# Kernel optimization log

Hardware: AMD Instinct MI355X
Metric: run time of the kernel (lower is better)

Reference implementation:

```python
import jax, jax.numpy as jnp
import numpy as np

EPS = 1e-5

def _layer_norm(x, g, b):
    mu = jnp.mean(x, axis=-1, keepdims=True)
    var = jnp.mean(jnp.square(x - mu), axis=-1, keepdims=True)
    return (x - mu) * jax.lax.rsqrt(var + EPS) * g + b

def setup_inputs() -> dict:
    key = jax.random.key(0)
    ks = jax.random.split(key, 8)
    B, N, M = 4, 2048, 2048
    Dq, Dc = 512, 768
    H, Dh = 8, 64
    inner = H * Dh  # 512
    s = lambda d: 1.0 / np.sqrt(d)
    return {
        "x": jax.random.normal(ks[0], (B, N, Dq), jnp.float32),
        "cond": jax.random.normal(ks[1], (B, M, Dc), jnp.float32),
        "lnx_g": jnp.ones((Dq,), jnp.float32),
        "lnx_b": jnp.zeros((Dq,), jnp.float32),
        "lnc_g": jnp.ones((Dc,), jnp.float32),
        "lnc_b": jnp.zeros((Dc,), jnp.float32),
        "Wq": jax.random.normal(ks[2], (Dq, inner), jnp.float32) * s(Dq),
        "Wk": jax.random.normal(ks[3], (Dc, inner), jnp.float32) * s(Dc),
        "Wv": jax.random.normal(ks[4], (Dc, inner), jnp.float32) * s(Dc),
        "Wo": jax.random.normal(ks[5], (inner, Dq), jnp.float32) * s(inner),
        "bo": jnp.zeros((Dq,), jnp.float32),
        "lnf_g": jnp.ones((Dq,), jnp.float32),
        "lnf_b": jnp.zeros((Dq,), jnp.float32),
    }

def reference(x, cond, lnx_g, lnx_b, lnc_g, lnc_b, Wq, Wk, Wv, Wo, bo, lnf_g, lnf_b):
    H = 8
    B, N, _ = x.shape
    M = cond.shape[1]
    x_orig = x
    xn = _layer_norm(x, lnx_g, lnx_b)
    cn = _layer_norm(cond, lnc_g, lnc_b)
    q = (xn @ Wq).reshape(B, N, H, -1).transpose(0, 2, 1, 3)  # b h n d
    k = (cn @ Wk).reshape(B, M, H, -1).transpose(0, 2, 1, 3)  # b h m d
    v = (cn @ Wv).reshape(B, M, H, -1).transpose(0, 2, 1, 3)
    scale = q.shape[-1] ** -0.5
    sim = jnp.einsum('bhid,bhjd->bhij', q, k) * scale
    attn = jax.nn.softmax(sim, axis=-1)
    out = jnp.einsum('bhij,bhjd->bhid', attn, v)
    out = out.transpose(0, 2, 1, 3).reshape(B, N, -1)  # b n (h d)
    out = out @ Wo + bo
    out = out + x_orig  # residual=True
    return _layer_norm(out, lnf_g, lnf_b)
```

## Files before the change

### kernel.cpp

```cpp
#include <hip/hip_runtime.h>
#include <hip/hip_bf16.h>
#include <math.h>

#define BB 4
#define NN 2048
#define MM 2048
#define DQ 512
#define DC 768
#define NH 8
#define DH 64
#define INNER 512
#define KVS 1024

typedef short bf16x8 __attribute__((ext_vector_type(8)));
typedef float f32x4  __attribute__((ext_vector_type(4)));

__device__ inline short fbf(float f) {
    __hip_bfloat16 h = __float2bfloat16(f);
    return __builtin_bit_cast(short, h);
}

__device__ inline void gld16(const void* gptr, void* lds_uniform_base) {
    __builtin_amdgcn_global_load_lds(
        (const __attribute__((address_space(1))) void*)gptr,
        (__attribute__((address_space(3))) void*)lds_uniform_base, 16, 0, 0);
}

__global__ __launch_bounds__(256) void prep_k(
    const float* __restrict__ x, const float* __restrict__ cond,
    const float* __restrict__ gx, const float* __restrict__ bx_,
    const float* __restrict__ gc, const float* __restrict__ bc,
    short* __restrict__ xn, short* __restrict__ cn,
    const float* __restrict__ Wq, const float* __restrict__ Wk,
    const float* __restrict__ Wv, const float* __restrict__ Wo,
    short* __restrict__ Wqt, short* __restrict__ Wkvt, short* __restrict__ Wot)
{
    const int bxid = blockIdx.x;
    const int t = threadIdx.x;

    if (bxid < 16384) {
        const int which = bxid >> 13;
        const int row   = bxid & 8191;
        const float* in = which ? cond : x;
        const float* g  = which ? gc : gx;
        const float* bb = which ? bc : bx_;
        short* out      = which ? cn : xn;
        const int D     = which ? DC : DQ;

        const float* xr = in + (size_t)row * D;
        float s = 0.f, s2 = 0.f;
        for (int d = t; d < D; d += 256) {
            float v = xr[d];
            s += v; s2 += v * v;
        }
        __shared__ float red[2][4];
        #pragma unroll
        for (int off = 32; off; off >>= 1) {
            s  += __shfl_down(s,  off, 64);
            s2 += __shfl_down(s2, off, 64);
        }
        const int wave = t >> 6, lane = t & 63;
        if (lane == 0) { red[0][wave] = s; red[1][wave] = s2; }
        __syncthreads();
        if (t == 0) {
            float ts = red[0][0] + red[0][1] + red[0][2] + red[0][3];
            float t2 = red[1][0] + red[1][1] + red[1][2] + red[1][3];
            float mu = ts / (float)D;
            float var = t2 / (float)D - mu * mu;
            red[0][0] = mu;
            red[1][0] = rsqrtf(var + 1e-5f);
        }
        __syncthreads();
        const float mu = red[0][0], rstd = red[1][0];
        short* o = out + (size_t)row * D;
        for (int d = t; d < D; d += 256)
            o[d] = fbf((xr[d] - mu) * rstd * g[d] + bb[d]);
    } else {
        const int tb = bxid - 16384;
        const int y = tb >> 4;
        const int n0 = (tb & 15) * 32;
        const float* W; short* Wt; int K, k0;
        if (y < 16)      { W = Wq; Wt = Wqt;  K = DQ; k0 = y * 32; }
        else if (y < 40) { W = Wk; Wt = Wkvt; K = DC; k0 = (y - 16) * 32; }
        else if (y < 64) { W = Wv; Wt = Wkvt + (size_t)512 * DC; K = DC; k0 = (y - 40) * 32; }
        else             { W = Wo; Wt = Wot;  K = DQ; k0 = (y - 64) * 32; }

        __shared__ float tile[32][33];
        const int r = t >> 3, c4 = (t & 7) * 4;
        float4 vv = *(const float4*)&W[(size_t)(k0 + r) * 512 + n0 + c4];
        tile[c4 + 0][r] = vv.x; tile[c4 + 1][r] = vv.y;
        tile[c4 + 2][r] = vv.z; tile[c4 + 3][r] = vv.w;
        __syncthreads();
        short4 sv;
        sv.x = fbf(tile[r][c4 + 0]); sv.y = fbf(tile[r][c4 + 1]);
        sv.z = fbf(tile[r][c4 + 2]); sv.w = fbf(tile[r][c4 + 3]);
        *(short4*)&Wt[(size_t)(n0 + r) * K + k0 + c4] = sv;
    }
}

__global__ __launch_bounds__(256) void layernorm_res_f32(
    const short* __restrict__ ob, const float* __restrict__ x,
    const float* __restrict__ g, const float* __restrict__ b,
    float* __restrict__ out)
{
    const int row = blockIdx.x;
    const int t = threadIdx.x;
    const size_t base = (size_t)row * DQ;
    float v0, v1;
    {
        unsigned u0 = (unsigned)(unsigned short)ob[base + t];
        unsigned u1 = (unsigned)(unsigned short)ob[base + t + 256];
        v0 = __builtin_bit_cast(float, u0 << 16) + x[base + t];
        v1 = __builtin_bit_cast(float, u1 << 16) + x[base + t + 256];
    }
    float s = v0 + v1, s2 = v0 * v0 + v1 * v1;
    __shared__ float red[2][4];
    #pragma unroll
    for (int off = 32; off; off >>= 1) {
        s  += __shfl_down(s,  off, 64);
        s2 += __shfl_down(s2, off, 64);
    }
    const int wave = t >> 6, lane = t & 63;
    if (lane == 0) { red[0][wave] = s; red[1][wave] = s2; }
    __syncthreads();
    if (t == 0) {
        float ts = red[0][0] + red[0][1] + red[0][2] + red[0][3];
        float t2 = red[1][0] + red[1][1] + red[1][2] + red[1][3];
        float mu = ts / (float)DQ;
        float var = t2 / (float)DQ - mu * mu;
        red[0][0] = mu;
        red[1][0] = rsqrtf(var + 1e-5f);
    }
    __syncthreads();
    const float mu = red[0][0], rstd = red[1][0];
    out[base + t]       = (v0 - mu) * rstd * g[t]       + b[t];
    out[base + t + 256] = (v1 - mu) * rstd * g[t + 256] + b[t + 256];
}

#define GBK 32

__global__ __launch_bounds__(256) void qkv_gemm(
    const short* __restrict__ xn, const short* __restrict__ cn,
    const short* __restrict__ Wqt, const short* __restrict__ Wkvt,
    short* __restrict__ qb, short* __restrict__ kvb, float qsc)
{
    const short* A; const short* Bt; short* outp; int K, Nout, n0; float sc;
    if (blockIdx.x < 4) {
        A = xn; Bt = Wqt; outp = qb; K = DQ; Nout = 512;
        n0 = blockIdx.x * 128; sc = qsc;
    } else {
        A = cn; Bt = Wkvt; outp = kvb; K = DC; Nout = 1024;
        n0 = (blockIdx.x - 4) * 128; sc = 1.f;
    }
    __shared__ short As[128 * GBK];
    __shared__ short Bs[128 * GBK];
    const int t = threadIdx.x;
    const int w = t >> 6, lane = t & 63;
    const int quad = lane >> 4, l16 = lane & 15;
    const int m0 = blockIdx.y * 128;
    const int wm = (w >> 1) * 64, wn = (w & 1) * 64;

    f32x4 acc[4][4];
    #pragma unroll
    for (int i = 0; i < 4; ++i)
        #pragma unroll
        for (int j = 0; j < 4; ++j) acc[i][j] = (f32x4){0.f, 0.f, 0.f, 0.f};

    for (int kt = 0; kt < K; kt += GBK) {
        __syncthreads();
        #pragma unroll
        for (int i = 0; i < 2; ++i) {
            const int j = w * 2 + i;
            const int c = j * 64 + lane;
            gld16(&A[(size_t)(m0 + (c >> 2)) * K + kt + (c & 3) * 8],
                  (char*)As + j * 1024);
            gld16(&Bt[(size_t)(n0 + (c >> 2)) * K + kt + (c & 3) * 8],
                  (char*)Bs + j * 1024);
        }
        __syncthreads();

        bf16x8 af[4], bfr[4];
        #pragma unroll
        for (int mt = 0; mt < 4; ++mt)
            af[mt] = *(bf16x8*)&As[(wm + mt * 16 + l16) * GBK + quad * 8];
        #pragma unroll
        for (int nt = 0; nt < 4; ++nt)
            bfr[nt] = *(bf16x8*)&Bs[(wn + nt * 16 + l16) * GBK + quad * 8];
        #pragma unroll
        for (int mt = 0; mt < 4; ++mt)
            #pragma unroll
            for (int nt = 0; nt < 4; ++nt)
                acc[mt][nt] = __builtin_amdgcn_mfma_f32_16x16x32_bf16(
                    af[mt], bfr[nt], acc[mt][nt], 0, 0, 0);
    }

    #pragma unroll
    for (int mt = 0; mt < 4; ++mt)
        #pragma unroll
        for (int r = 0; r < 4; ++r) {
            const int m = m0 + wm + mt * 16 + quad * 4 + r;
            #pragma unroll
            for (int nt = 0; nt < 4; ++nt) {
                const int n = n0 + wn + nt * 16 + l16;
                outp[(size_t)m * Nout + n] = fbf(acc[mt][nt][r] * sc);
            }
        }
}

__global__ __launch_bounds__(256) void oproj_gemm(
    const short* __restrict__ A, const short* __restrict__ Bt,
    short* __restrict__ outb, const float* __restrict__ bias)
{
    const int K = INNER, Nout = INNER;
    __shared__ short As[128 * GBK];
    __shared__ short Bs[64 * GBK];
    const int t = threadIdx.x;
    const int w = t >> 6, lane = t & 63;
    const int quad = lane >> 4, l16 = lane & 15;
    const int m0 = blockIdx.y * 128, n0 = blockIdx.x * 64;
    const int wm = (w >> 1) * 64, wn = (w & 1) * 32;

    f32x4 acc[4][2];
    #pragma unroll
    for (int i = 0; i < 4; ++i)
        #pragma unroll
        for (int j = 0; j < 2; ++j) acc[i][j] = (f32x4){0.f, 0.f, 0.f, 0.f};

    for (int kt = 0; kt < K; kt += GBK) {
        __syncthreads();
        #pragma unroll
        for (int i = 0; i < 2; ++i) {
            const int j = w * 2 + i;
            const int c = j * 64 + lane;
            gld16(&A[(size_t)(m0 + (c >> 2)) * K + kt + (c & 3) * 8],
                  (char*)As + j * 1024);
        }
        {
            const int c = w * 64 + lane;
            gld16(&Bt[(size_t)(n0 + (c >> 2)) * K + kt + (c & 3) * 8],
                  (char*)Bs + w * 1024);
        }
        __syncthreads();

        bf16x8 af[4], bfr[2];
        #pragma unroll
        for (int mt = 0; mt < 4; ++mt)
            af[mt] = *(bf16x8*)&As[(wm + mt * 16 + l16) * GBK + quad * 8];
        #pragma unroll
        for (int nt = 0; nt < 2; ++nt)
            bfr[nt] = *(bf16x8*)&Bs[(wn + nt * 16 + l16) * GBK + quad * 8];
        #pragma unroll
        for (int mt = 0; mt < 4; ++mt)
            #pragma unroll
            for (int nt = 0; nt < 2; ++nt)
                acc[mt][nt] = __builtin_amdgcn_mfma_f32_16x16x32_bf16(
                    af[mt], bfr[nt], acc[mt][nt], 0, 0, 0);
    }

    #pragma unroll
    for (int mt = 0; mt < 4; ++mt)
        #pragma unroll
        for (int r = 0; r < 4; ++r) {
            const int m = m0 + wm + mt * 16 + quad * 4 + r;
            #pragma unroll
            for (int nt = 0; nt < 2; ++nt) {
                const int n = n0 + wn + nt * 16 + l16;
                outb[(size_t)m * Nout + n] = fbf(acc[mt][nt][r] + bias[n]);
            }
        }
}

#define QT 128
#define JT 64
#define KSTR 72
#define MH (MM / 2)
#define NIT (MH / JT)

__global__ __launch_bounds__(512) void attention_mfma(
    const short* __restrict__ q, const short* __restrict__ kv,
    short* __restrict__ o)
{
    const int b = blockIdx.z, h = blockIdx.y;
    const int i0 = blockIdx.x * QT;
    const int t = threadIdx.x;
    const int wave = t >> 6, lane = t & 63;
    const int w4 = wave & 3, hh = wave >> 2;
    const int quad = lane >> 4, l16 = lane & 15;

    __shared__ __align__(16) char smem[73728];
    typedef short KT[2][64][KSTR];
    KT* Ks = (KT*)smem;
    KT* Vt = (KT*)(smem + 36864);
    float (*Obuf)[32][68] = (float(*)[32][68])(smem);
    float (*Lbuf)[32]     = (float(*)[32])(smem + 34816);

    bf16x8 qf[2][2];
    #pragma unroll
    for (int it = 0; it < 2; ++it) {
        const int row = i0 + w4 * 32 + it * 16 + l16;
        const short* qp = &q[((size_t)(b * NN + row)) * INNER + h * DH];
        qf[it][0] = *(const bf16x8*)&qp[quad * 8];
        qf[it][1] = *(const bf16x8*)&qp[32 + quad * 8];
    }

    f32x4 Oa[2][4];
    f32x4 La[2];
    #pragma unroll
    for (int it = 0; it < 2; ++it) {
        La[it] = (f32x4){0.f, 0.f, 0.f, 0.f};
        #pragma unroll
        for (int dt = 0; dt < 4; ++dt) Oa[it][dt] = (f32x4){0.f, 0.f, 0.f, 0.f};
    }

    const bf16x8 ones8 = {(short)0x3F80, (short)0x3F80, (short)0x3F80, (short)0x3F80,
                          (short)0x3F80, (short)0x3F80, (short)0x3F80, (short)0x3F80};

    const int tt = t & 255, th = t >> 8;
    const int kjj = tt >> 3, kdq = (tt & 7) * 8;
    const int vjp = tt & 31, vd0 = (tt >> 5) * 8;

    const int jl0 = 2 * vjp;
    const int vcol = (jl0 >> 5) * 32 + (((jl0 >> 2) & 3) * 8)
                   + (((jl0 >> 4) & 1) * 4) + (jl0 & 3);

    const short* kp0 = kv + ((size_t)(b * MM + th * MH + kjj))      * KVS + h * DH + kdq;
    const short* kp1 = kv + ((size_t)(b * MM + th * MH + kjj + 32)) * KVS + h * DH + kdq;
    const short* vp0 = kv + ((size_t)(b * MM + th * MH + jl0))      * KVS + 512 + h * DH + vd0;
    const short* vp1 = vp0 + KVS;

    bf16x8 ka, kb2, va, vb;
    auto load = [&]() {
        ka  = *(const bf16x8*)kp0;
        kb2 = *(const bf16x8*)kp1;
        va  = *(const bf16x8*)vp0;
        vb  = *(const bf16x8*)vp1;
        kp0 += (size_t)JT * KVS; kp1 += (size_t)JT * KVS;
        vp0 += (size_t)JT * KVS; vp1 += (size_t)JT * KVS;
    };
    auto store = [&](int pb) {
        *(bf16x8*)&Ks[pb][th][kjj][kdq]      = ka;
        *(bf16x8*)&Ks[pb][th][kjj + 32][kdq] = kb2;
        #pragma unroll
        for (int i = 0; i < 8; ++i) {
            short2 pr; pr.x = va[i]; pr.y = vb[i];
            *(short2*)&Vt[pb][th][vd0 + i][vcol] = pr;
        }
    };

    load(); store(0);
    __syncthreads();

    for (int itr = 0; itr < NIT; ++itr) {
        const int p = itr & 1;
        const bool more = (itr + 1 < NIT);
        if (more) load();

        #pragma unroll
        for (int cc = 0; cc < 2; ++cc) {
            f32x4 Sc[2][2];
            #pragma unroll
            for (int jtl = 0; jtl < 2; ++jtl) {
                const int jt = cc * 2 + jtl;
                bf16x8 kf0 = *(bf16x8*)&Ks[p][hh][jt * 16 + l16][quad * 8];
                bf16x8 kf1 = *(bf16x8*)&Ks[p][hh][jt * 16 + l16][32 + quad * 8];
                #pragma unroll
                for (int it = 0; it < 2; ++it) {
                    f32x4 c = (f32x4){0.f, 0.f, 0.f, 0.f};
                    c = __builtin_amdgcn_mfma_f32_16x16x32_bf16(kf0, qf[it][0], c, 0, 0, 0);
                    c = __builtin_amdgcn_mfma_f32_16x16x32_bf16(kf1, qf[it][1], c, 0, 0, 0);
                    Sc[jtl][it] = c;
                }
            }

            bf16x8 p8[2];
            #pragma unroll
            for (int it = 0; it < 2; ++it) {
                const float e0 = exp2f(Sc[0][it][0]), e1 = exp2f(Sc[0][it][1]);
                const float e2 = exp2f(Sc[0][it][2]), e3 = exp2f(Sc[0][it][3]);
                const float f0 = exp2f(Sc[1][it][0]), f1 = exp2f(Sc[1][it][1]);
                const float f2 = exp2f(Sc[1][it][2]), f3 = exp2f(Sc[1][it][3]);
                uint4 pk;
                pk.x = __builtin_amdgcn_perm(__builtin_bit_cast(unsigned, e1),
                                             __builtin_bit_cast(unsigned, e0), 0x07060302u);
                pk.y = __builtin_amdgcn_perm(__builtin_bit_cast(unsigned, e3),
                                             __builtin_bit_cast(unsigned, e2), 0x07060302u);
                pk.z = __builtin_amdgcn_perm(__builtin_bit_cast(unsigned, f1),
                                             __builtin_bit_cast(unsigned, f0), 0x07060302u);
                pk.w = __builtin_amdgcn_perm(__builtin_bit_cast(unsigned, f3),
                                             __builtin_bit_cast(unsigned, f2), 0x07060302u);
                p8[it] = __builtin_bit_cast(bf16x8, pk);
            }

            #pragma unroll
            for (int dt = 0; dt < 4; ++dt) {
                bf16x8 vb8 = *(bf16x8*)&Vt[p][hh][dt * 16 + l16][cc * 32 + quad * 8];
                Oa[0][dt] = __builtin_amdgcn_mfma_f32_16x16x32_bf16(p8[0], vb8, Oa[0][dt], 0, 0, 0);
                Oa[1][dt] = __builtin_amdgcn_mfma_f32_16x16x32_bf16(p8[1], vb8, Oa[1][dt], 0, 0, 0);
            }
            La[0] = __builtin_amdgcn_mfma_f32_16x16x32_bf16(p8[0], ones8, La[0], 0, 0, 0);
            La[1] = __builtin_amdgcn_mfma_f32_16x16x32_bf16(p8[1], ones8, La[1], 0, 0, 0);
        }

        if (more) store(p ^ 1);
        __syncthreads();
    }

    if (wave >= 4) {
        #pragma unroll
        for (int it = 0; it < 2; ++it) {
            #pragma unroll
            for (int r = 0; r < 4; ++r) {
                const int qr = it * 16 + quad * 4 + r;
                #pragma unroll
                for (int dt = 0; dt < 4; ++dt)
                    Obuf[w4][qr][dt * 16 + l16] = Oa[it][dt][r];
                if (l16 == 0) Lbuf[w4][qr] = La[it][r];
            }
        }
    }
    __syncthreads();
    if (wave < 4) {
        #pragma unroll
        for (int it = 0; it < 2; ++it) {
            #pragma unroll
            for (int r = 0; r < 4; ++r) {
                const int qr = it * 16 + quad * 4 + r;
                const float ltot = La[it][r] + Lbuf[w4][qr];
                const float inv = 1.f / ltot;
                const int row = i0 + w4 * 32 + qr;
                #pragma unroll
                for (int dt = 0; dt < 4; ++dt) {
                    const float val = Oa[it][dt][r] + Obuf[w4][qr][dt * 16 + l16];
                    o[((size_t)(b * NN + row)) * INNER + h * DH + dt * 16 + l16] =
                        fbf(val * inv);
                }
            }
        }
    }
}

extern "C" void kernel_launch(void* const* d_in, const int* in_sizes, int n_in,
                              void* d_out, int out_size, void* d_ws, size_t ws_size,
                              hipStream_t stream)
{
    const float* x     = (const float*)d_in[0];
    const float* cond  = (const float*)d_in[1];
    const float* lnx_g = (const float*)d_in[2];
    const float* lnx_b = (const float*)d_in[3];
    const float* lnc_g = (const float*)d_in[4];
    const float* lnc_b = (const float*)d_in[5];
    const float* Wq    = (const float*)d_in[6];
    const float* Wk    = (const float*)d_in[7];
    const float* Wv    = (const float*)d_in[8];
    const float* Wo    = (const float*)d_in[9];
    const float* bo    = (const float*)d_in[10];
    const float* lnf_g = (const float*)d_in[11];
    const float* lnf_b = (const float*)d_in[12];
    float* out = (float*)d_out;
    char* ws = (char*)d_ws;

    const int R = BB * NN;

    short* xn_bf  = (short*)(ws);
    short* cn_bf  = (short*)(ws + (8u << 20));
    short* Wq_t   = (short*)(ws + (20u << 20));
    short* Wo_t   = (short*)(ws + (21u << 20));
    short* Wkv_t  = (short*)(ws + (22u << 20));
    short* qb     = (short*)(ws + (24u << 20));
    short* kvb    = (short*)(ws + (32u << 20));
    short* ab     = (short*)(ws + (48u << 20));
    short* ob     = (short*)(ws + (56u << 20));

    prep_k<<<17664, 256, 0, stream>>>(
        x, cond, lnx_g, lnx_b, lnc_g, lnc_b, xn_bf, cn_bf,
        Wq, Wk, Wv, Wo, Wq_t, Wkv_t, Wo_t);

    qkv_gemm<<<dim3(12, R / 128), 256, 0, stream>>>(
        xn_bf, cn_bf, Wq_t, Wkv_t, qb, kvb, 0.125f * 1.44269504089f);

    attention_mfma<<<dim3(NN / QT, NH, BB), 512, 0, stream>>>(qb, kvb, ab);

    oproj_gemm<<<dim3(INNER / 64, R / 128), 256, 0, stream>>>(ab, Wo_t, ob, bo);

    layernorm_res_f32<<<R, 256, 0, stream>>>(ob, x, lnf_g, lnf_b, out);
}
```

Before: 225.1 us.

## Restructure attention with direct global-to-LDS loads, transposed LDS reads, smaller tiles

Rewrites the attention kernel to stage K and V straight from global memory into LDS with global_load_lds, using an XOR-swizzled K layout. V fragments are read with ds_read_b64_tr_b16 instead of being transposed in registers through scalar LDS writes. Query and key tiles shrink to 64x32, LDS drops to 32KB and launch bounds request higher occupancy. A 1D grid is remapped so consecutive blocks spread across heads and batches. The aim is to remove the register round-trip and bank-conflicted transpose stores, at the cost of less reuse per block and more barriers per unit of work.

After: 226.3 us. Within noise of the previous version (+0.5%).

```diff
diff --git a/kernel.cpp b/kernel.cpp
--- a/kernel.cpp
+++ b/kernel.cpp
@@ -13,6 +13,7 @@
 #define KVS 1024
 
 typedef short bf16x8 __attribute__((ext_vector_type(8)));
+typedef short bf16x4 __attribute__((ext_vector_type(4)));
 typedef float f32x4  __attribute__((ext_vector_type(4)));
 
 __device__ inline short fbf(float f) {
@@ -270,170 +271,163 @@
         }
 }
 
-#define QT 128
-#define JT 64
-#define KSTR 72
+#define QT 64
+#define JT 32
 #define MH (MM / 2)
 #define NIT (MH / JT)
-
-__global__ __launch_bounds__(512) void attention_mfma(
+#define ABUF 16384
+
+__global__ __launch_bounds__(512, 6) void attention_mfma(
     const short* __restrict__ q, const short* __restrict__ kv,
     short* __restrict__ o)
 {
-    const int b = blockIdx.z, h = blockIdx.y;
-    const int i0 = blockIdx.x * QT;
+    const int bid = blockIdx.x;
+    const int wg  = (bid & 7) * 128 + (bid >> 3);
+    const int ib  = wg & 31;
+    const int bh  = wg >> 5;
+    const int h   = bh & 7, b = bh >> 3;
+    const int i0  = ib * QT;
+
     const int t = threadIdx.x;
     const int wave = t >> 6, lane = t & 63;
     const int w4 = wave & 3, hh = wave >> 2;
     const int quad = lane >> 4, l16 = lane & 15;
 
-    __shared__ __align__(16) char smem[73728];
-    typedef short KT[2][64][KSTR];
-    KT* Ks = (KT*)smem;
-    KT* Vt = (KT*)(smem + 36864);
-    float (*Obuf)[32][68] = (float(*)[32][68])(smem);
-    float (*Lbuf)[32]     = (float(*)[32])(smem + 34816);
-
-    bf16x8 qf[2][2];
-    #pragma unroll
-    for (int it = 0; it < 2; ++it) {
-        const int row = i0 + w4 * 32 + it * 16 + l16;
-        const short* qp = &q[((size_t)(b * NN + row)) * INNER + h * DH];
-        qf[it][0] = *(const bf16x8*)&qp[quad * 8];
-        qf[it][1] = *(const bf16x8*)&qp[32 + quad * 8];
-    }
-
-    f32x4 Oa[2][4];
-    f32x4 La[2];
-    #pragma unroll
-    for (int it = 0; it < 2; ++it) {
-        La[it] = (f32x4){0.f, 0.f, 0.f, 0.f};
-        #pragma unroll
-        for (int dt = 0; dt < 4; ++dt) Oa[it][dt] = (f32x4){0.f, 0.f, 0.f, 0.f};
-    }
+    __shared__ __align__(16) char smem[2 * ABUF];
+
+    const int qrow = i0 + w4 * 16 + l16;
+    const short* qp = &q[((size_t)(b * NN + qrow)) * INNER + h * DH];
+    const bf16x8 qf0 = *(const bf16x8*)&qp[quad * 8];
+    const bf16x8 qf1 = *(const bf16x8*)&qp[32 + quad * 8];
+
+    f32x4 Oa[4];
+    f32x4 La = (f32x4){0.f, 0.f, 0.f, 0.f};
+    #pragma unroll
+    for (int dt = 0; dt < 4; ++dt) Oa[dt] = (f32x4){0.f, 0.f, 0.f, 0.f};
 
     const bf16x8 ones8 = {(short)0x3F80, (short)0x3F80, (short)0x3F80, (short)0x3F80,
                           (short)0x3F80, (short)0x3F80, (short)0x3F80, (short)0x3F80};
 
-    const int tt = t & 255, th = t >> 8;
-    const int kjj = tt >> 3, kdq = (tt & 7) * 8;
-    const int vjp = tt & 31, vd0 = (tt >> 5) * 8;
-
-    const int jl0 = 2 * vjp;
-    const int vcol = (jl0 >> 5) * 32 + (((jl0 >> 2) & 3) * 8)
-                   + (((jl0 >> 4) & 1) * 4) + (jl0 & 3);
-
-    const short* kp0 = kv + ((size_t)(b * MM + th * MH + kjj))      * KVS + h * DH + kdq;
-    const short* kp1 = kv + ((size_t)(b * MM + th * MH + kjj + 32)) * KVS + h * DH + kdq;
-    const short* vp0 = kv + ((size_t)(b * MM + th * MH + jl0))      * KVS + 512 + h * DH + vd0;
-    const short* vp1 = vp0 + KVS;
-
-    bf16x8 ka, kb2, va, vb;
-    auto load = [&]() {
-        ka  = *(const bf16x8*)kp0;
-        kb2 = *(const bf16x8*)kp1;
-        va  = *(const bf16x8*)vp0;
-        vb  = *(const bf16x8*)vp1;
-        kp0 += (size_t)JT * KVS; kp1 += (size_t)JT * KVS;
-        vp0 += (size_t)JT * KVS; vp1 += (size_t)JT * KVS;
+    const int kr = w4 * 8 + (lane >> 3);
+    const int kc = ((lane & 7) ^ (lane >> 3)) * 8;
+    const short* kp = kv + ((size_t)(b * MM + hh * MH + kr)) * KVS + h * DH + kc;
+    const int vj = (lane >> 3) * 4 + ((lane & 7) >> 1);
+    const int vd = w4 * 16 + (lane & 1) * 8;
+    const short* vp = kv + ((size_t)(b * MM + hh * MH + vj)) * KVS + 512 + h * DH + vd;
+    const size_t ADV = (size_t)JT * KVS;
+
+    char* const kdst = smem + hh * 4096 + w4 * 1024;
+    char* const vdst = smem + 8192 + hh * 4096 + w4 * 1024;
+
+    const char* const Kh0 = smem + hh * 4096;
+    const int koffA = l16 * 128 + ((quad ^ (l16 & 7)) * 16);
+    const int koffB = koffA ^ 64;
+    const unsigned vbase =
+        (unsigned)(size_t)(__attribute__((address_space(3))) char*)(smem + 8192 + hh * 4096)
+        + (unsigned)(lane * 8);
+
+    auto stage = [&](int pb) {
+        gld16(kp, kdst + pb);
+        gld16(vp, vdst + pb);
+        kp += ADV; vp += ADV;
     };
-    auto store = [&](int pb) {
-        *(bf16x8*)&Ks[pb][th][kjj][kdq]      = ka;
-        *(bf16x8*)&Ks[pb][th][kjj + 32][kdq] = kb2;
-        #pragma unroll
-        for (int i = 0; i < 8; ++i) {
-            short2 pr; pr.x = va[i]; pr.y = vb[i];
-            *(short2*)&Vt[pb][th][vd0 + i][vcol] = pr;
-        }
+
+    auto compute = [&](int pb) {
+        const char* Kh = Kh0 + pb;
+        bf16x8 kf0 = *(const bf16x8*)(Kh + koffA);
+        bf16x8 kf1 = *(const bf16x8*)(Kh + koffB);
+        bf16x8 kg0 = *(const bf16x8*)(Kh + koffA + 2048);
+        bf16x8 kg1 = *(const bf16x8*)(Kh + koffB + 2048);
+        f32x4 Sc0 = (f32x4){0.f, 0.f, 0.f, 0.f};
+        f32x4 Sc1 = (f32x4){0.f, 0.f, 0.f, 0.f};
+        Sc0 = __builtin_amdgcn_mfma_f32_16x16x32_bf16(kf0, qf0, Sc0, 0, 0, 0);
+        Sc0 = __builtin_amdgcn_mfma_f32_16x16x32_bf16(kf1, qf1, Sc0, 0, 0, 0);
+        Sc1 = __builtin_amdgcn_mfma_f32_16x16x32_bf16(kg0, qf0, Sc1, 0, 0, 0);
+        Sc1 = __builtin_amdgcn_mfma_f32_16x16x32_bf16(kg1, qf1, Sc1, 0, 0, 0);
+
+        bf16x4 ta0, tb0, ta1, tb1, ta2, tb2, ta3, tb3;
+        {
+            const unsigned va = vbase + (unsigned)pb;
+            asm volatile(
+                "ds_read_b64_tr_b16 %0, %8 offset:0\n\t"
+                "ds_read_b64_tr_b16 %1, %8 offset:512\n\t"
+                "ds_read_b64_tr_b16 %2, %8 offset:1024\n\t"
+                "ds_read_b64_tr_b16 %3, %8 offset:1536\n\t"
+                "ds_read_b64_tr_b16 %4, %8 offset:2048\n\t"
+                "ds_read_b64_tr_b16 %5, %8 offset:2560\n\t"
+                "ds_read_b64_tr_b16 %6, %8 offset:3072\n\t"
+                "ds_read_b64_tr_b16 %7, %8 offset:3584"
+                : "=&v"(ta0), "=&v"(tb0), "=&v"(ta1), "=&v"(tb1),
+                  "=&v"(ta2), "=&v"(tb2), "=&v"(ta3), "=&v"(tb3)
+                : "v"(va));
+        }
+
+        const float e0 = exp2f(Sc0[0]), e1 = exp2f(Sc0[1]);
+        const float e2 = exp2f(Sc0[2]), e3 = exp2f(Sc0[3]);
+        const float f0 = exp2f(Sc1[0]), f1 = exp2f(Sc1[1]);
+        const float f2 = exp2f(Sc1[2]), f3 = exp2f(Sc1[3]);
+        uint4 pk;
+        pk.x = __builtin_amdgcn_perm(__builtin_bit_cast(unsigned, e1),
+                                     __builtin_bit_cast(unsigned, e0), 0x07060302u);
+        pk.y = __builtin_amdgcn_perm(__builtin_bit_cast(unsigned, e3),
+                                     __builtin_bit_cast(unsigned, e2), 0x07060302u);
+        pk.z = __builtin_amdgcn_perm(__builtin_bit_cast(unsigned, f1),
+                                     __builtin_bit_cast(unsigned, f0), 0x07060302u);
+        pk.w = __builtin_amdgcn_perm(__builtin_bit_cast(unsigned, f3),
+                                     __builtin_bit_cast(unsigned, f2), 0x07060302u);
+        const bf16x8 p8 = __builtin_bit_cast(bf16x8, pk);
+
+        asm volatile("s_waitcnt lgkmcnt(0)" ::: "memory");
+        __builtin_amdgcn_sched_barrier(0);
+
+        const bf16x8 v0 = __builtin_shufflevector(ta0, tb0, 0, 1, 2, 3, 4, 5, 6, 7);
+        const bf16x8 v1 = __builtin_shufflevector(ta1, tb1, 0, 1, 2, 3, 4, 5, 6, 7);
+        const bf16x8 v2 = __builtin_shufflevector(ta2, tb2, 0, 1, 2, 3, 4, 5, 6, 7);
+        const bf16x8 v3 = __builtin_shufflevector(ta3, tb3, 0, 1, 2, 3, 4, 5, 6, 7);
+        Oa[0] = __builtin_amdgcn_mfma_f32_16x16x32_bf16(p8, v0, Oa[0], 0, 0, 0);
+        Oa[1] = __builtin_amdgcn_mfma_f32_16x16x32_bf16(p8, v1, Oa[1], 0, 0, 0);
+        Oa[2] = __builtin_amdgcn_mfma_f32_16x16x32_bf16(p8, v2, Oa[2], 0, 0, 0);
+        Oa[3] = __builtin_amdgcn_mfma_f32_16x16x32_bf16(p8, v3, Oa[3], 0, 0, 0);
+        La    = __builtin_amdgcn_mfma_f32_16x16x32_bf16(p8, ones8, La, 0, 0, 0);
     };
 
-    load(); store(0);
+    stage(0);
     __syncthreads();
 
-    for (int itr = 0; itr < NIT; ++itr) {
-        const int p = itr & 1;
-        const bool more = (itr + 1 < NIT);
-        if (more) load();
-
-        #pragma unroll
-        for (int cc = 0; cc < 2; ++cc) {
-            f32x4 Sc[2][2];
-            #pragma unroll
-            for (int jtl = 0; jtl < 2; ++jtl) {
-                const int jt = cc * 2 + jtl;
-                bf16x8 kf0 = *(bf16x8*)&Ks[p][hh][jt * 16 + l16][quad * 8];
-                bf16x8 kf1 = *(bf16x8*)&Ks[p][hh][jt * 16 + l16][32 + quad * 8];
-                #pragma unroll
-                for (int it = 0; it < 2; ++it) {
-                    f32x4 c = (f32x4){0.f, 0.f, 0.f, 0.f};
-                    c = __builtin_amdgcn_mfma_f32_16x16x32_bf16(kf0, qf[it][0], c, 0, 0, 0);
-                    c = __builtin_amdgcn_mfma_f32_16x16x32_bf16(kf1, qf[it][1], c, 0, 0, 0);
-                    Sc[jtl][it] = c;
-                }
-            }
-
-            bf16x8 p8[2];
-            #pragma unroll
-            for (int it = 0; it < 2; ++it) {
-                const float e0 = exp2f(Sc[0][it][0]), e1 = exp2f(Sc[0][it][1]);
-                const float e2 = exp2f(Sc[0][it][2]), e3 = exp2f(Sc[0][it][3]);
-                const float f0 = exp2f(Sc[1][it][0]), f1 = exp2f(Sc[1][it][1]);
-                const float f2 = exp2f(Sc[1][it][2]), f3 = exp2f(Sc[1][it][3]);
-                uint4 pk;
-                pk.x = __builtin_amdgcn_perm(__builtin_bit_cast(unsigned, e1),
-                                             __builtin_bit_cast(unsigned, e0), 0x07060302u);
-                pk.y = __builtin_amdgcn_perm(__builtin_bit_cast(unsigned, e3),
-                                             __builtin_bit_cast(unsigned, e2), 0x07060302u);
-                pk.z = __builtin_amdgcn_perm(__builtin_bit_cast(unsigned, f1),
-                                             __builtin_bit_cast(unsigned, f0), 0x07060302u);
-                pk.w = __builtin_amdgcn_perm(__builtin_bit_cast(unsigned, f3),
-                                             __builtin_bit_cast(unsigned, f2), 0x07060302u);
-                p8[it] = __builtin_bit_cast(bf16x8, pk);
-            }
-
+    for (int itr = 0; itr < NIT; itr += 2) {
+        stage(ABUF);
+        compute(0);
+        __syncthreads();
+        if (itr + 2 < NIT) stage(0);
+        compute(ABUF);
+        __syncthreads();
+    }
+
+    float (*Obuf)[16][68] = (float (*)[16][68])smem;
+    float (*Lbuf)[16]     = (float (*)[16])(smem + 17408);
+    if (hh == 1) {
+        #pragma unroll
+        for (int r = 0; r < 4; ++r) {
+            const int qr = quad * 4 + r;
+            #pragma unroll
+            for (int dt = 0; dt < 4; ++dt)
+                Obuf[w4][qr][dt * 16 + l16] = Oa[dt][r];
+            if (l16 == 0) Lbuf[w4][qr] = La[r];
+        }
+    }
+    __syncthreads();
+    if (hh == 0) {
+        #pragma unroll
+        for (int r = 0; r < 4; ++r) {
+            const int qr = quad * 4 + r;
+            const float ltot = La[r] + Lbuf[w4][qr];
+            const float inv = 1.f / ltot;
+            const int row = i0 + w4 * 16 + qr;
             #pragma unroll
             for (int dt = 0; dt < 4; ++dt) {
-                bf16x8 vb8 = *(bf16x8*)&Vt[p][hh][dt * 16 + l16][cc * 32 + quad * 8];
-                Oa[0][dt] = __builtin_amdgcn_mfma_f32_16x16x32_bf16(p8[0], vb8, Oa[0][dt], 0, 0, 0);
-                Oa[1][dt] = __builtin_amdgcn_mfma_f32_16x16x32_bf16(p8[1], vb8, Oa[1][dt], 0, 0, 0);
-            }
-            La[0] = __builtin_amdgcn_mfma_f32_16x16x32_bf16(p8[0], ones8, La[0], 0, 0, 0);
-            La[1] = __builtin_amdgcn_mfma_f32_16x16x32_bf16(p8[1], ones8, La[1], 0, 0, 0);
-        }
-
-        if (more) store(p ^ 1);
-        __syncthreads();
-    }
-
-    if (wave >= 4) {
-        #pragma unroll
-        for (int it = 0; it < 2; ++it) {
-            #pragma unroll
-            for (int r = 0; r < 4; ++r) {
-                const int qr = it * 16 + quad * 4 + r;
-                #pragma unroll
-                for (int dt = 0; dt < 4; ++dt)
-                    Obuf[w4][qr][dt * 16 + l16] = Oa[it][dt][r];
-                if (l16 == 0) Lbuf[w4][qr] = La[it][r];
-            }
-        }
-    }
-    __syncthreads();
-    if (wave < 4) {
-        #pragma unroll
-        for (int it = 0; it < 2; ++it) {
-            #pragma unroll
-            for (int r = 0; r < 4; ++r) {
-                const int qr = it * 16 + quad * 4 + r;
-                const float ltot = La[it][r] + Lbuf[w4][qr];
-                const float inv = 1.f / ltot;
-                const int row = i0 + w4 * 32 + qr;
-                #pragma unroll
-                for (int dt = 0; dt < 4; ++dt) {
-                    const float val = Oa[it][dt][r] + Obuf[w4][qr][dt * 16 + l16];
-                    o[((size_t)(b * NN + row)) * INNER + h * DH + dt * 16 + l16] =
-                        fbf(val * inv);
-                }
+                const float val = Oa[dt][r] + Obuf[w4][qr][dt * 16 + l16];
+                o[((size_t)(b * NN + row)) * INNER + h * DH + dt * 16 + l16] =
+                    fbf(val * inv);
             }
         }
     }
@@ -478,7 +472,7 @@
     qkv_gemm<<<dim3(12, R / 128), 256, 0, stream>>>(
         xn_bf, cn_bf, Wq_t, Wkv_t, qb, kvb, 0.125f * 1.44269504089f);
 
-    attention_mfma<<<dim3(NN / QT, NH, BB), 512, 0, stream>>>(qb, kvb, ab);
+    attention_mfma<<<dim3(BB * NH * (NN / QT)), 512, 0, stream>>>(qb, kvb, ab);
 
     oproj_gemm<<<dim3(INNER / 64, R / 128), 256, 0, stream>>>(ab, Wo_t, ob, bo);
 
```
